# Kernel tuning notes

Hardware: AMD Instinct MI355X
Metric: run time of the kernel (lower is better)

Reference implementation:

```python
import jax, jax.numpy as jnp
import numpy as np

# Model config (matches init_kwargs)
E, TOP_K, H, I = 16, 2, 2048, 1024
B, S = 2, 2048
GROUP = 16                 # NVFP4 quantization group size along contraction dim
RSF = 1.0                  # routed_scaling_factor


def setup_inputs() -> dict:
    key = jax.random.key(0)
    ks = jax.random.split(key, 6)
    hidden_states = jax.random.normal(ks[0], (B, S, H), dtype=jnp.float32)
    gate_weight = jax.random.normal(ks[1], (E, H), dtype=jnp.float32) * 0.02
    # int4 codes stored as int32 in [0,16); reference subtracts 8 -> [-8,7]
    fc_up_qweights = jax.random.randint(ks[2], (E, H, I), 0, 16, dtype=jnp.int32)
    fc_up_blocks_scale = jax.random.uniform(ks[3], (E, H // GROUP, I), dtype=jnp.float32) * 0.02
    fc_up_global_scale = jnp.ones((1,), dtype=jnp.float32)
    fc_down_qweights = jax.random.randint(ks[4], (E, I, H), 0, 16, dtype=jnp.int32)
    fc_down_blocks_scale = jax.random.uniform(ks[5], (E, I // GROUP, H), dtype=jnp.float32) * 0.02
    fc_down_global_scale = jnp.ones((1,), dtype=jnp.float32)
    return {
        'hidden_states': hidden_states,
        'gate_weight': gate_weight,
        'fc_up_blocks_scale': fc_up_blocks_scale,
        'fc_up_global_scale': fc_up_global_scale,
        'fc_down_blocks_scale': fc_down_blocks_scale,
        'fc_down_global_scale': fc_down_global_scale,
        'fc_up_qweights': fc_up_qweights,
        'fc_down_qweights': fc_down_qweights,
    }


def _dequant(q, blocks_scale, global_scale):
    # q: [E,K,N] int codes (0..15 -> -8..7); blocks_scale: [E,K/GROUP,N]
    e, k, n = q.shape
    w = (q.astype(jnp.float32) - 8.0).reshape(e, k // GROUP, GROUP, n)
    w = w * blocks_scale[:, :, None, :]
    return w.reshape(e, k, n) * global_scale[0]


def reference(hidden_states, gate_weight, fc_up_blocks_scale, fc_up_global_scale,
              fc_down_blocks_scale, fc_down_global_scale,
              fc_up_qweights, fc_down_qweights):
    b, s, h = hidden_states.shape
    x = hidden_states.reshape(-1, h).astype(jnp.float32)          # [T,H]
    t = x.shape[0]

    # Router: HF sigmoid routing mapped through logsigmoid so that
    # softmax(logsigmoid(l)) == sigmoid(l)/sum(sigmoid(l))  (nemotron_h_plugin_router_logits)
    logits = jax.nn.log_sigmoid(x @ gate_weight.T)                # [T,E]
    probs = jax.nn.softmax(logits, axis=-1)
    topw, topi = jax.lax.top_k(probs, TOP_K)                      # [T,K]
    topw = topw / (jnp.sum(topw, axis=-1, keepdims=True) + 1e-20) # renormalize

    # Dense per-token expert weights [T,E] (scatter of top-k weights)
    wdense = jnp.zeros((t, E), dtype=jnp.float32)
    wdense = wdense.at[jnp.arange(t)[:, None], topi].add(topw) * RSF

    w_up = _dequant(fc_up_qweights, fc_up_blocks_scale, fc_up_global_scale)     # [E,H,I]
    w_down = _dequant(fc_down_qweights, fc_down_blocks_scale, fc_down_global_scale)  # [E,I,H]

    z = jnp.einsum('th,ehi->tei', x, w_up)                        # up proj
    a = jnp.square(jnp.maximum(z, 0.0))                           # activation_type=0: ReLU^2
    aw = a * wdense[:, :, None]                                   # fold routing weights (linear)
    y = jnp.einsum('tei,eih->th', aw, w_down)                     # down proj + combine
    return y.reshape(b, s, h)
```

## Files before the change

kernel.cpp:

```cpp
#include <hip/hip_runtime.h>

#define TOK 4096
#define NE 16
#define HD 2048
#define ID 1024
#define QGROUP 16
#define CAP 4096

typedef _Float16 half4v __attribute__((ext_vector_type(4)));
typedef _Float16 half8v __attribute__((ext_vector_type(8)));
typedef float float4v __attribute__((ext_vector_type(4)));

__device__ __forceinline__ float bf2f(unsigned int u) { return __uint_as_float(u << 16); }

__global__ __launch_bounds__(256) void prep_kernel(
    const float* __restrict__ x, _Float16* __restrict__ xh)
{
    int i8 = (blockIdx.x * 256 + threadIdx.x) * 8;
    float4 f0 = *(const float4*)&x[i8];
    float4 f1 = *(const float4*)&x[i8 + 4];
    half8v h;
    h[0] = (_Float16)f0.x; h[1] = (_Float16)f0.y; h[2] = (_Float16)f0.z; h[3] = (_Float16)f0.w;
    h[4] = (_Float16)f1.x; h[5] = (_Float16)f1.y; h[6] = (_Float16)f1.z; h[7] = (_Float16)f1.w;
    *(half8v*)&xh[i8] = h;
}

__global__ __launch_bounds__(256) void router_kernel(
    const float* __restrict__ x, const float* __restrict__ gw,
    int* __restrict__ counts, int* __restrict__ pair_row, float* __restrict__ pair_w)
{
    int t = blockIdx.x;
    int tid = threadIdx.x;
    float p[NE];
#pragma unroll
    for (int e = 0; e < NE; e++) p[e] = 0.f;
    const float* xr = x + (size_t)t * HD;
    for (int h = tid; h < HD; h += 256) {
        float xv = xr[h];
#pragma unroll
        for (int e = 0; e < NE; e++) p[e] = fmaf(xv, gw[e * HD + h], p[e]);
    }
#pragma unroll
    for (int off = 32; off > 0; off >>= 1) {
#pragma unroll
        for (int e = 0; e < NE; e++) p[e] += __shfl_down(p[e], off, 64);
    }
    __shared__ float part[4][NE];
    int wave = tid >> 6, lane = tid & 63;
    if (lane == 0) {
#pragma unroll
        for (int e = 0; e < NE; e++) part[wave][e] = p[e];
    }
    __syncthreads();
    if (tid == 0) {
        float s[NE]; float sum = 0.f;
#pragma unroll
        for (int e = 0; e < NE; e++) {
            float l = part[0][e] + part[1][e] + part[2][e] + part[3][e];
            float sg = 1.f / (1.f + expf(-l));
            s[e] = sg; sum += sg;
        }
        int i1 = 0;
#pragma unroll
        for (int e = 1; e < NE; e++) if (s[e] > s[i1]) i1 = e;
        int i2 = (i1 == 0) ? 1 : 0;
#pragma unroll
        for (int e = 0; e < NE; e++) if (e != i1 && s[e] > s[i2]) i2 = e;
        float p1 = s[i1] / sum, p2 = s[i2] / sum;
        float inv = 1.f / (p1 + p2 + 1e-20f);
        float w1 = p1 * inv, w2 = p2 * inv;
        int s1 = atomicAdd(&counts[i1], 1);
        pair_row[i1 * CAP + s1] = t * 2;     pair_w[i1 * CAP + s1] = w1;
        int s2 = atomicAdd(&counts[i2], 1);
        pair_row[i2 * CAP + s2] = t * 2 + 1; pair_w[i2 * CAP + s2] = w2;
    }
}

template<int N, int K, bool UP>
__global__ __launch_bounds__(256) void gemm_kernel(
    const _Float16* __restrict__ A, const int* __restrict__ qw,
    const float* __restrict__ bsc, const float* __restrict__ gsc,
    const int* __restrict__ counts, const int* __restrict__ pair_row,
    const float* __restrict__ pair_w,
    _Float16* __restrict__ store16, float* __restrict__ store32)
{
    constexpr int NT = N / 128;
    const int e = blockIdx.y;
    const int cnt = counts[e];
    const int mt = blockIdx.x / NT, nt = blockIdx.x % NT;
    const int mbase = mt * 128;
    if (mbase >= cnt) return;
    const int nbase = nt * 128;
    const int tid = threadIdx.x;

    __shared__ _Float16 As[128][40];
    __shared__ _Float16 Bs[128][40];
    __shared__ int rows_s[128];
    __shared__ float pw_s[128];

    if (tid < 128) {
        int idx = mbase + tid; if (idx >= cnt) idx = cnt - 1;
        rows_s[tid] = pair_row[e * CAP + idx];
        pw_s[tid] = UP ? pair_w[e * CAP + idx] : 0.f;
    }

    const int lane = tid & 63, wv = tid >> 6;
    const int quad = lane >> 4, lm = lane & 15;
    const int wr = (wv >> 1) * 64, wc = (wv & 1) * 64;

    float4v acc[4][4];
#pragma unroll
    for (int mi = 0; mi < 4; mi++)
#pragma unroll
        for (int ni = 0; ni < 4; ni++) acc[mi][ni] = (float4v){0.f, 0.f, 0.f, 0.f};

    const int am = tid & 127, akk = (tid >> 7) * 16;
    const int bn4 = (tid & 31) * 4, bkb = (tid >> 5) * 4;

    for (int k0 = 0; k0 < K; k0 += 32) {
        __syncthreads();
        {
            int pr = rows_s[am];
            int row = UP ? (pr >> 1) : pr;
            const _Float16* src = A + (size_t)row * K + k0 + akk;
            uint4 r0 = *(const uint4*)src;
            uint4 r1 = *(const uint4*)(src + 8);
            *(uint4*)&As[am][akk] = r0;
            *(uint4*)&As[am][akk + 8] = r1;
        }
        {
            const int kabs = k0 + bkb;
            const int g = kabs >> 4;
            const float4 sc = *(const float4*)&bsc[((size_t)e * (K / QGROUP) + g) * N + nbase + bn4];
            const int4 c0 = *(const int4*)&qw[((size_t)e * K + kabs + 0) * N + nbase + bn4];
            const int4 c1 = *(const int4*)&qw[((size_t)e * K + kabs + 1) * N + nbase + bn4];
            const int4 c2 = *(const int4*)&qw[((size_t)e * K + kabs + 2) * N + nbase + bn4];
            const int4 c3 = *(const int4*)&qw[((size_t)e * K + kabs + 3) * N + nbase + bn4];
            half4v q;
            q[0] = (_Float16)((c0.x - 8) * sc.x); q[1] = (_Float16)((c1.x - 8) * sc.x);
            q[2] = (_Float16)((c2.x - 8) * sc.x); q[3] = (_Float16)((c3.x - 8) * sc.x);
            *(half4v*)&Bs[bn4 + 0][bkb] = q;
            q[0] = (_Float16)((c0.y - 8) * sc.y); q[1] = (_Float16)((c1.y - 8) * sc.y);
            q[2] = (_Float16)((c2.y - 8) * sc.y); q[3] = (_Float16)((c3.y - 8) * sc.y);
            *(half4v*)&Bs[bn4 + 1][bkb] = q;
            q[0] = (_Float16)((c0.z - 8) * sc.z); q[1] = (_Float16)((c1.z - 8) * sc.z);
            q[2] = (_Float16)((c2.z - 8) * sc.z); q[3] = (_Float16)((c3.z - 8) * sc.z);
            *(half4v*)&Bs[bn4 + 2][bkb] = q;
            q[0] = (_Float16)((c0.w - 8) * sc.w); q[1] = (_Float16)((c1.w - 8) * sc.w);
            q[2] = (_Float16)((c2.w - 8) * sc.w); q[3] = (_Float16)((c3.w - 8) * sc.w);
            *(half4v*)&Bs[bn4 + 3][bkb] = q;
        }
        __syncthreads();
        half8v af[4], bf[4];
#pragma unroll
        for (int mi = 0; mi < 4; mi++)
            af[mi] = *(const half8v*)&As[wr + mi * 16 + lm][quad * 8];
#pragma unroll
        for (int ni = 0; ni < 4; ni++)
            bf[ni] = *(const half8v*)&Bs[wc + ni * 16 + lm][quad * 8];
#pragma unroll
        for (int mi = 0; mi < 4; mi++)
#pragma unroll
            for (int ni = 0; ni < 4; ni++)
                acc[mi][ni] = __builtin_amdgcn_mfma_f32_16x16x32_f16(af[mi], bf[ni], acc[mi][ni], 0, 0, 0);
    }

    const float gs = gsc[0];
#pragma unroll
    for (int mi = 0; mi < 4; mi++) {
#pragma unroll
        for (int r = 0; r < 4; r++) {
            const int rl = wr + mi * 16 + quad * 4 + r;
            const int grow = mbase + rl;
            if (grow < cnt) {
                const int pr = rows_s[rl];
#pragma unroll
                for (int ni = 0; ni < 4; ni++) {
                    const int col = nbase + wc + ni * 16 + lm;
                    float v = acc[mi][ni][r] * gs;
                    if (UP) {
                        v = fmaxf(v, 0.f);
                        v = v * v * pw_s[rl];
                        store16[(size_t)pr * N + col] = (_Float16)v;
                    } else if (store16) {
                        store16[(size_t)pr * N + col] = (_Float16)v;
                    } else {
                        atomicAdd(&store32[(size_t)(pr >> 1) * N + col], v);
                    }
                }
            }
        }
    }
}

__global__ __launch_bounds__(256) void finalize_kernel(
    const _Float16* __restrict__ ydown, float* __restrict__ out)
{
    int i = (blockIdx.x * 256 + threadIdx.x) * 4;
    int t = i >> 11;
    int h = i & 2047;
    size_t a = ((size_t)t << 12) + h;
    half4v ra = *(const half4v*)&ydown[a];
    half4v rb = *(const half4v*)&ydown[a + HD];
    float4 o;
    o.x = (float)ra[0] + (float)rb[0];
    o.y = (float)ra[1] + (float)rb[1];
    o.z = (float)ra[2] + (float)rb[2];
    o.w = (float)ra[3] + (float)rb[3];
    *(float4*)&out[i] = o;
}

extern "C" void kernel_launch(void* const* d_in, const int* in_sizes, int n_in,
                              void* d_out, int out_size, void* d_ws, size_t ws_size,
                              hipStream_t stream) {
    const float* x   = (const float*)d_in[0];
    const float* gw  = (const float*)d_in[1];
    const float* usc = (const float*)d_in[2];
    const float* ugs = (const float*)d_in[3];
    const float* dsc = (const float*)d_in[4];
    const float* dgs = (const float*)d_in[5];
    const int*   uq  = (const int*)d_in[6];
    const int*   dq  = (const int*)d_in[7];
    float* out = (float*)d_out;

    char* ws = (char*)d_ws;
    int*   counts   = (int*)(ws + 0);
    int*   pair_row = (int*)(ws + 4096);
    float* pair_w   = (float*)(ws + 4096 + (size_t)NE * CAP * 4);
    _Float16* xh    = (_Float16*)(ws + 528384);
    _Float16* act   = (_Float16*)(ws + 528384 + (size_t)TOK * HD * 2);
    _Float16* ydown = (_Float16*)(ws + 528384 + (size_t)TOK * HD * 2
                                  + (size_t)2 * TOK * ID * 2);
    const size_t need_ydown = 34082816ull + (size_t)2 * TOK * HD * 2;
    const bool use_ydown = ws_size >= need_ydown;

    hipMemsetAsync(counts, 0, 4096, stream);
    if (!use_ydown) hipMemsetAsync(out, 0, (size_t)TOK * HD * 4, stream);

    prep_kernel<<<(TOK * HD) / (256 * 8), 256, 0, stream>>>(x, xh);
    router_kernel<<<TOK, 256, 0, stream>>>(x, gw, counts, pair_row, pair_w);
    gemm_kernel<ID, HD, true><<<dim3((CAP / 128) * (ID / 128), NE), 256, 0, stream>>>(
        xh, uq, usc, ugs, counts, pair_row, pair_w, act, nullptr);
    gemm_kernel<HD, ID, false><<<dim3((CAP / 128) * (HD / 128), NE), 256, 0, stream>>>(
        act, dq, dsc, dgs, counts, pair_row, pair_w,
        use_ydown ? ydown : nullptr, use_ydown ? nullptr : out);
    if (use_ydown)
        finalize_kernel<<<(TOK * HD) / 1024, 256, 0, stream>>>(ydown, out);
}
```

Baseline: 605.4 us.

## Prefetch next K-tile into registers and reshape grouped GEMM tiles to 64x128x64

The grouped MoE GEMM now loads the next K-step's activations, int4 codes and scales into registers before running the current step's MFMAs, so global latency overlaps compute. The tile changes from 128x128 with K-step 32 to 64 rows by 128 columns with K-step 64, and the grid is doubled along M. Each thread now dequantizes 8 K values per column and writes them as half8 vectors. In exchange, each weight tile is reloaded by twice as many blocks, and register pressure rises from the prefetch buffers.

```diff
diff --git a/kernel.cpp b/kernel.cpp
--- a/kernel.cpp
+++ b/kernel.cpp
@@ -10,8 +10,6 @@
 typedef _Float16 half4v __attribute__((ext_vector_type(4)));
 typedef _Float16 half8v __attribute__((ext_vector_type(8)));
 typedef float float4v __attribute__((ext_vector_type(4)));
-
-__device__ __forceinline__ float bf2f(unsigned int u) { return __uint_as_float(u << 16); }
 
 __global__ __launch_bounds__(256) void prep_kernel(
     const float* __restrict__ x, _Float16* __restrict__ xh)
@@ -88,95 +86,109 @@
     const int e = blockIdx.y;
     const int cnt = counts[e];
     const int mt = blockIdx.x / NT, nt = blockIdx.x % NT;
-    const int mbase = mt * 128;
+    const int mbase = mt * 64;
     if (mbase >= cnt) return;
     const int nbase = nt * 128;
     const int tid = threadIdx.x;
 
-    __shared__ _Float16 As[128][40];
-    __shared__ _Float16 Bs[128][40];
-    __shared__ int rows_s[128];
-    __shared__ float pw_s[128];
-
-    if (tid < 128) {
+    __shared__ _Float16 As[64][68];
+    __shared__ _Float16 Bs[128][68];
+    __shared__ int rows_s[64];
+    __shared__ float pw_s[64];
+
+    if (tid < 64) {
         int idx = mbase + tid; if (idx >= cnt) idx = cnt - 1;
         rows_s[tid] = pair_row[e * CAP + idx];
         pw_s[tid] = UP ? pair_w[e * CAP + idx] : 0.f;
     }
+    __syncthreads();
+
+    const int arow = tid & 63;
+    const int aseg = (tid >> 6) * 16;
+    const int pr_a = rows_s[arow];
+    const _Float16* asrc = A + (size_t)(UP ? (pr_a >> 1) : pr_a) * K + aseg;
+
+    const int bn4 = (tid & 31) * 4;
+    const int bkb = (tid >> 5) * 8;
+    const int* bsrc = qw + ((size_t)e * K + bkb) * N + nbase + bn4;
+    const float* ssrc = bsc + ((size_t)e * (K / QGROUP) + (bkb >> 4)) * N + nbase + bn4;
+
+    uint4 pa0 = *(const uint4*)asrc;
+    uint4 pa1 = *(const uint4*)(asrc + 8);
+    int4 pc[8];
+#pragma unroll
+    for (int j = 0; j < 8; j++) pc[j] = *(const int4*)(bsrc + (size_t)j * N);
+    float4 psc = *(const float4*)ssrc;
 
     const int lane = tid & 63, wv = tid >> 6;
     const int quad = lane >> 4, lm = lane & 15;
-    const int wr = (wv >> 1) * 64, wc = (wv & 1) * 64;
-
-    float4v acc[4][4];
-#pragma unroll
-    for (int mi = 0; mi < 4; mi++)
+    const int wm = (wv & 1) * 32, wn = (wv >> 1) * 64;
+
+    float4v acc[2][4];
+#pragma unroll
+    for (int mi = 0; mi < 2; mi++)
 #pragma unroll
         for (int ni = 0; ni < 4; ni++) acc[mi][ni] = (float4v){0.f, 0.f, 0.f, 0.f};
 
-    const int am = tid & 127, akk = (tid >> 7) * 16;
-    const int bn4 = (tid & 31) * 4, bkb = (tid >> 5) * 4;
-
-    for (int k0 = 0; k0 < K; k0 += 32) {
+    for (int k0 = 0; k0 < K; k0 += 64) {
         __syncthreads();
+        *(uint4*)&As[arow][aseg] = pa0;
+        *(uint4*)&As[arow][aseg + 8] = pa1;
         {
-            int pr = rows_s[am];
-            int row = UP ? (pr >> 1) : pr;
-            const _Float16* src = A + (size_t)row * K + k0 + akk;
-            uint4 r0 = *(const uint4*)src;
-            uint4 r1 = *(const uint4*)(src + 8);
-            *(uint4*)&As[am][akk] = r0;
-            *(uint4*)&As[am][akk + 8] = r1;
-        }
-        {
-            const int kabs = k0 + bkb;
-            const int g = kabs >> 4;
-            const float4 sc = *(const float4*)&bsc[((size_t)e * (K / QGROUP) + g) * N + nbase + bn4];
-            const int4 c0 = *(const int4*)&qw[((size_t)e * K + kabs + 0) * N + nbase + bn4];
-            const int4 c1 = *(const int4*)&qw[((size_t)e * K + kabs + 1) * N + nbase + bn4];
-            const int4 c2 = *(const int4*)&qw[((size_t)e * K + kabs + 2) * N + nbase + bn4];
-            const int4 c3 = *(const int4*)&qw[((size_t)e * K + kabs + 3) * N + nbase + bn4];
-            half4v q;
-            q[0] = (_Float16)((c0.x - 8) * sc.x); q[1] = (_Float16)((c1.x - 8) * sc.x);
-            q[2] = (_Float16)((c2.x - 8) * sc.x); q[3] = (_Float16)((c3.x - 8) * sc.x);
-            *(half4v*)&Bs[bn4 + 0][bkb] = q;
-            q[0] = (_Float16)((c0.y - 8) * sc.y); q[1] = (_Float16)((c1.y - 8) * sc.y);
-            q[2] = (_Float16)((c2.y - 8) * sc.y); q[3] = (_Float16)((c3.y - 8) * sc.y);
-            *(half4v*)&Bs[bn4 + 1][bkb] = q;
-            q[0] = (_Float16)((c0.z - 8) * sc.z); q[1] = (_Float16)((c1.z - 8) * sc.z);
-            q[2] = (_Float16)((c2.z - 8) * sc.z); q[3] = (_Float16)((c3.z - 8) * sc.z);
-            *(half4v*)&Bs[bn4 + 2][bkb] = q;
-            q[0] = (_Float16)((c0.w - 8) * sc.w); q[1] = (_Float16)((c1.w - 8) * sc.w);
-            q[2] = (_Float16)((c2.w - 8) * sc.w); q[3] = (_Float16)((c3.w - 8) * sc.w);
-            *(half4v*)&Bs[bn4 + 3][bkb] = q;
+            half8v h0, h1, h2, h3;
+#pragma unroll
+            for (int j = 0; j < 8; j++) {
+                h0[j] = (_Float16)((float)(pc[j].x - 8) * psc.x);
+                h1[j] = (_Float16)((float)(pc[j].y - 8) * psc.y);
+                h2[j] = (_Float16)((float)(pc[j].z - 8) * psc.z);
+                h3[j] = (_Float16)((float)(pc[j].w - 8) * psc.w);
+            }
+            *(half8v*)&Bs[bn4 + 0][bkb] = h0;
+            *(half8v*)&Bs[bn4 + 1][bkb] = h1;
+            *(half8v*)&Bs[bn4 + 2][bkb] = h2;
+            *(half8v*)&Bs[bn4 + 3][bkb] = h3;
         }
         __syncthreads();
-        half8v af[4], bf[4];
-#pragma unroll
-        for (int mi = 0; mi < 4; mi++)
-            af[mi] = *(const half8v*)&As[wr + mi * 16 + lm][quad * 8];
-#pragma unroll
-        for (int ni = 0; ni < 4; ni++)
-            bf[ni] = *(const half8v*)&Bs[wc + ni * 16 + lm][quad * 8];
-#pragma unroll
-        for (int mi = 0; mi < 4; mi++)
+        if (k0 + 64 < K) {
+            asrc += 64;
+            pa0 = *(const uint4*)asrc;
+            pa1 = *(const uint4*)(asrc + 8);
+            bsrc += (size_t)64 * N;
+#pragma unroll
+            for (int j = 0; j < 8; j++) pc[j] = *(const int4*)(bsrc + (size_t)j * N);
+            ssrc += (size_t)4 * N;
+            psc = *(const float4*)ssrc;
+        }
+        half8v af[2][2], bf[2][4];
+#pragma unroll
+        for (int ks = 0; ks < 2; ks++) {
+#pragma unroll
+            for (int mi = 0; mi < 2; mi++)
+                af[ks][mi] = *(const half8v*)&As[wm + mi * 16 + lm][ks * 32 + quad * 8];
 #pragma unroll
             for (int ni = 0; ni < 4; ni++)
-                acc[mi][ni] = __builtin_amdgcn_mfma_f32_16x16x32_f16(af[mi], bf[ni], acc[mi][ni], 0, 0, 0);
+                bf[ks][ni] = *(const half8v*)&Bs[wn + ni * 16 + lm][ks * 32 + quad * 8];
+        }
+#pragma unroll
+        for (int ks = 0; ks < 2; ks++)
+#pragma unroll
+            for (int mi = 0; mi < 2; mi++)
+#pragma unroll
+                for (int ni = 0; ni < 4; ni++)
+                    acc[mi][ni] = __builtin_amdgcn_mfma_f32_16x16x32_f16(af[ks][mi], bf[ks][ni], acc[mi][ni], 0, 0, 0);
     }
 
     const float gs = gsc[0];
 #pragma unroll
-    for (int mi = 0; mi < 4; mi++) {
+    for (int mi = 0; mi < 2; mi++) {
 #pragma unroll
         for (int r = 0; r < 4; r++) {
-            const int rl = wr + mi * 16 + quad * 4 + r;
-            const int grow = mbase + rl;
-            if (grow < cnt) {
+            const int rl = wm + mi * 16 + quad * 4 + r;
+            if (mbase + rl < cnt) {
                 const int pr = rows_s[rl];
 #pragma unroll
                 for (int ni = 0; ni < 4; ni++) {
-                    const int col = nbase + wc + ni * 16 + lm;
+                    const int col = nbase + wn + ni * 16 + lm;
                     float v = acc[mi][ni][r] * gs;
                     if (UP) {
                         v = fmaxf(v, 0.f);
@@ -239,9 +251,9 @@
 
     prep_kernel<<<(TOK * HD) / (256 * 8), 256, 0, stream>>>(x, xh);
     router_kernel<<<TOK, 256, 0, stream>>>(x, gw, counts, pair_row, pair_w);
-    gemm_kernel<ID, HD, true><<<dim3((CAP / 128) * (ID / 128), NE), 256, 0, stream>>>(
+    gemm_kernel<ID, HD, true><<<dim3((CAP / 64) * (ID / 128), NE), 256, 0, stream>>>(
         xh, uq, usc, ugs, counts, pair_row, pair_w, act, nullptr);
-    gemm_kernel<HD, ID, false><<<dim3((CAP / 128) * (HD / 128), NE), 256, 0, stream>>>(
+    gemm_kernel<HD, ID, false><<<dim3((CAP / 64) * (HD / 128), NE), 256, 0, stream>>>(
         act, dq, dsc, dgs, counts, pair_row, pair_w,
         use_ydown ? ydown : nullptr, use_ydown ? nullptr : out);
     if (use_ydown)
```

Result: slower. 635.1 us (+4.9%).

## Pre-dequantize weights to transposed fp16 and stream tiles via global_load_lds

Applied to the files above, without the earlier changes.

Adds a separate kernel that dequantizes each expert's int32 int4 codes into a transposed fp16 weight buffer in workspace, one projection at a time. A new GEMM then loads A and B tiles with direct global-to-LDS 16-byte loads instead of dequantizing inside the main loop. The down projection now always accumulates into the output with fp32 atomics, replacing the fp16 per-pair buffer and its finalize pass. This trades an extra full pass over the weights (read int32, write fp16) for a much leaner GEMM inner loop. The new path has no LDS padding and no double buffering, so bank conflicts and load latency may still limit it.

```diff
diff --git a/kernel.cpp b/kernel.cpp
--- a/kernel.cpp
+++ b/kernel.cpp
@@ -11,7 +11,11 @@
 typedef _Float16 half8v __attribute__((ext_vector_type(8)));
 typedef float float4v __attribute__((ext_vector_type(4)));
 
-__device__ __forceinline__ float bf2f(unsigned int u) { return __uint_as_float(u << 16); }
+__device__ __forceinline__ void g2l16(const void* g, void* l) {
+    __builtin_amdgcn_global_load_lds(
+        (const __attribute__((address_space(1))) unsigned int*)g,
+        (__attribute__((address_space(3))) unsigned int*)l, 16, 0, 0);
+}
 
 __global__ __launch_bounds__(256) void prep_kernel(
     const float* __restrict__ x, _Float16* __restrict__ xh)
@@ -76,10 +80,46 @@
     }
 }
 
+template<int K, int N>
+__global__ __launch_bounds__(256) void dequantT_kernel(
+    const int* __restrict__ qw, const float* __restrict__ bsc, _Float16* __restrict__ wq)
+{
+    const int e = blockIdx.z, kt = blockIdx.y, nt = blockIdx.x;
+    const int tid = threadIdx.x;
+    __shared__ _Float16 T[64][68];
+
+    const int c4 = (tid & 15) * 4;
+    const int r0 = tid >> 4;
+#pragma unroll
+    for (int p = 0; p < 4; p++) {
+        const int r = p * 16 + r0;
+        const int kabs = kt * 64 + r;
+        const int4 c = *(const int4*)&qw[((size_t)e * K + kabs) * N + nt * 64 + c4];
+        const float4 sc = *(const float4*)&bsc[((size_t)e * (K / QGROUP) + (kabs >> 4)) * N + nt * 64 + c4];
+        half4v h;
+        h[0] = (_Float16)((float)(c.x - 8) * sc.x);
+        h[1] = (_Float16)((float)(c.y - 8) * sc.y);
+        h[2] = (_Float16)((float)(c.z - 8) * sc.z);
+        h[3] = (_Float16)((float)(c.w - 8) * sc.w);
+        *(half4v*)&T[r][c4] = h;
+    }
+    __syncthreads();
+    const int nrow = tid >> 2;
+    const int kseg = (tid & 3) * 16;
+    half8v o0, o1;
+#pragma unroll
+    for (int i = 0; i < 8; i++) o0[i] = T[kseg + i][nrow];
+#pragma unroll
+    for (int i = 0; i < 8; i++) o1[i] = T[kseg + 8 + i][nrow];
+    _Float16* dst = wq + ((size_t)e * N + nt * 64 + nrow) * K + kt * 64 + kseg;
+    *(half8v*)dst = o0;
+    *(half8v*)(dst + 8) = o1;
+}
+
 template<int N, int K, bool UP>
-__global__ __launch_bounds__(256) void gemm_kernel(
-    const _Float16* __restrict__ A, const int* __restrict__ qw,
-    const float* __restrict__ bsc, const float* __restrict__ gsc,
+__global__ __launch_bounds__(256) void gemm2_kernel(
+    const _Float16* __restrict__ A, const _Float16* __restrict__ BT,
+    const float* __restrict__ gsc,
     const int* __restrict__ counts, const int* __restrict__ pair_row,
     const float* __restrict__ pair_w,
     _Float16* __restrict__ store16, float* __restrict__ store32)
@@ -93,6 +133,108 @@
     const int nbase = nt * 128;
     const int tid = threadIdx.x;
 
+    __shared__ _Float16 As[128 * 32];
+    __shared__ _Float16 Bs[128 * 32];
+    __shared__ int rows_s[128];
+    __shared__ float pw_s[128];
+
+    if (tid < 128) {
+        int idx = mbase + tid; if (idx >= cnt) idx = cnt - 1;
+        rows_s[tid] = pair_row[e * CAP + idx];
+        pw_s[tid] = UP ? pair_w[e * CAP + idx] : 0.f;
+    }
+    __syncthreads();
+
+    const int lane = tid & 63, wv = tid >> 6;
+    const int quad = lane >> 4, lm = lane & 15;
+    const int wr = (wv >> 1) * 64, wc = (wv & 1) * 64;
+
+    const int lsub = lane >> 2;
+    const int lkof = (lane & 3) * 8;
+    const _Float16* asrc[2];
+    const _Float16* bsrc[2];
+    _Float16* adst[2];
+    _Float16* bdst[2];
+#pragma unroll
+    for (int i = 0; i < 2; i++) {
+        const int lr = wv * 32 + i * 16 + lsub;
+        const int pr = rows_s[lr];
+        asrc[i] = A + (size_t)(UP ? (pr >> 1) : pr) * K + lkof;
+        bsrc[i] = BT + ((size_t)e * N + nbase + lr) * K + lkof;
+        adst[i] = &As[(wv * 32 + i * 16) * 32];
+        bdst[i] = &Bs[(wv * 32 + i * 16) * 32];
+    }
+
+    float4v acc[4][4];
+#pragma unroll
+    for (int mi = 0; mi < 4; mi++)
+#pragma unroll
+        for (int ni = 0; ni < 4; ni++) acc[mi][ni] = (float4v){0.f, 0.f, 0.f, 0.f};
+
+    for (int k0 = 0; k0 < K; k0 += 32) {
+#pragma unroll
+        for (int i = 0; i < 2; i++) {
+            g2l16(asrc[i] + k0, adst[i]);
+            g2l16(bsrc[i] + k0, bdst[i]);
+        }
+        __syncthreads();
+        half8v af[4], bf[4];
+#pragma unroll
+        for (int mi = 0; mi < 4; mi++)
+            af[mi] = *(const half8v*)&As[(wr + mi * 16 + lm) * 32 + quad * 8];
+#pragma unroll
+        for (int ni = 0; ni < 4; ni++)
+            bf[ni] = *(const half8v*)&Bs[(wc + ni * 16 + lm) * 32 + quad * 8];
+#pragma unroll
+        for (int mi = 0; mi < 4; mi++)
+#pragma unroll
+            for (int ni = 0; ni < 4; ni++)
+                acc[mi][ni] = __builtin_amdgcn_mfma_f32_16x16x32_f16(af[mi], bf[ni], acc[mi][ni], 0, 0, 0);
+        __syncthreads();
+    }
+
+    const float gs = gsc[0];
+#pragma unroll
+    for (int mi = 0; mi < 4; mi++) {
+#pragma unroll
+        for (int r = 0; r < 4; r++) {
+            const int rl = wr + mi * 16 + quad * 4 + r;
+            if (mbase + rl < cnt) {
+                const int pr = rows_s[rl];
+#pragma unroll
+                for (int ni = 0; ni < 4; ni++) {
+                    const int col = nbase + wc + ni * 16 + lm;
+                    float v = acc[mi][ni][r] * gs;
+                    if (UP) {
+                        v = fmaxf(v, 0.f);
+                        v = v * v * pw_s[rl];
+                        store16[(size_t)pr * N + col] = (_Float16)v;
+                    } else {
+                        atomicAdd(&store32[(size_t)(pr >> 1) * N + col], v);
+                    }
+                }
+            }
+        }
+    }
+}
+
+template<int N, int K, bool UP>
+__global__ __launch_bounds__(256) void gemm_fused_kernel(
+    const _Float16* __restrict__ A, const int* __restrict__ qw,
+    const float* __restrict__ bsc, const float* __restrict__ gsc,
+    const int* __restrict__ counts, const int* __restrict__ pair_row,
+    const float* __restrict__ pair_w,
+    _Float16* __restrict__ store16, float* __restrict__ store32)
+{
+    constexpr int NT = N / 128;
+    const int e = blockIdx.y;
+    const int cnt = counts[e];
+    const int mt = blockIdx.x / NT, nt = blockIdx.x % NT;
+    const int mbase = mt * 128;
+    if (mbase >= cnt) return;
+    const int nbase = nt * 128;
+    const int tid = threadIdx.x;
+
     __shared__ _Float16 As[128][40];
     __shared__ _Float16 Bs[128][40];
     __shared__ int rows_s[128];
@@ -121,17 +263,13 @@
         __syncthreads();
         {
             int pr = rows_s[am];
-            int row = UP ? (pr >> 1) : pr;
-            const _Float16* src = A + (size_t)row * K + k0 + akk;
-            uint4 r0 = *(const uint4*)src;
-            uint4 r1 = *(const uint4*)(src + 8);
-            *(uint4*)&As[am][akk] = r0;
-            *(uint4*)&As[am][akk + 8] = r1;
+            const _Float16* src = A + (size_t)(UP ? (pr >> 1) : pr) * K + k0 + akk;
+            *(uint4*)&As[am][akk] = *(const uint4*)src;
+            *(uint4*)&As[am][akk + 8] = *(const uint4*)(src + 8);
         }
         {
             const int kabs = k0 + bkb;
-            const int g = kabs >> 4;
-            const float4 sc = *(const float4*)&bsc[((size_t)e * (K / QGROUP) + g) * N + nbase + bn4];
+            const float4 sc = *(const float4*)&bsc[((size_t)e * (K / QGROUP) + (kabs >> 4)) * N + nbase + bn4];
             const int4 c0 = *(const int4*)&qw[((size_t)e * K + kabs + 0) * N + nbase + bn4];
             const int4 c1 = *(const int4*)&qw[((size_t)e * K + kabs + 1) * N + nbase + bn4];
             const int4 c2 = *(const int4*)&qw[((size_t)e * K + kabs + 2) * N + nbase + bn4];
@@ -171,8 +309,7 @@
 #pragma unroll
         for (int r = 0; r < 4; r++) {
             const int rl = wr + mi * 16 + quad * 4 + r;
-            const int grow = mbase + rl;
-            if (grow < cnt) {
+            if (mbase + rl < cnt) {
                 const int pr = rows_s[rl];
 #pragma unroll
                 for (int ni = 0; ni < 4; ni++) {
@@ -182,8 +319,6 @@
                         v = fmaxf(v, 0.f);
                         v = v * v * pw_s[rl];
                         store16[(size_t)pr * N + col] = (_Float16)v;
-                    } else if (store16) {
-                        store16[(size_t)pr * N + col] = (_Float16)v;
                     } else {
                         atomicAdd(&store32[(size_t)(pr >> 1) * N + col], v);
                     }
@@ -191,23 +326,6 @@
             }
         }
     }
-}
-
-__global__ __launch_bounds__(256) void finalize_kernel(
-    const _Float16* __restrict__ ydown, float* __restrict__ out)
-{
-    int i = (blockIdx.x * 256 + threadIdx.x) * 4;
-    int t = i >> 11;
-    int h = i & 2047;
-    size_t a = ((size_t)t << 12) + h;
-    half4v ra = *(const half4v*)&ydown[a];
-    half4v rb = *(const half4v*)&ydown[a + HD];
-    float4 o;
-    o.x = (float)ra[0] + (float)rb[0];
-    o.y = (float)ra[1] + (float)rb[1];
-    o.z = (float)ra[2] + (float)rb[2];
-    o.w = (float)ra[3] + (float)rb[3];
-    *(float4*)&out[i] = o;
 }
 
 extern "C" void kernel_launch(void* const* d_in, const int* in_sizes, int n_in,
@@ -229,21 +347,28 @@
     float* pair_w   = (float*)(ws + 4096 + (size_t)NE * CAP * 4);
     _Float16* xh    = (_Float16*)(ws + 528384);
     _Float16* act   = (_Float16*)(ws + 528384 + (size_t)TOK * HD * 2);
-    _Float16* ydown = (_Float16*)(ws + 528384 + (size_t)TOK * HD * 2
+    _Float16* wq    = (_Float16*)(ws + 528384 + (size_t)TOK * HD * 2
                                   + (size_t)2 * TOK * ID * 2);
-    const size_t need_ydown = 34082816ull + (size_t)2 * TOK * HD * 2;
-    const bool use_ydown = ws_size >= need_ydown;
+    const size_t need_deq = 34082816ull + (size_t)NE * HD * ID * 2;
+    const bool use_deq = ws_size >= need_deq;
 
     hipMemsetAsync(counts, 0, 4096, stream);
-    if (!use_ydown) hipMemsetAsync(out, 0, (size_t)TOK * HD * 4, stream);
+    hipMemsetAsync(out, 0, (size_t)TOK * HD * 4, stream);
 
     prep_kernel<<<(TOK * HD) / (256 * 8), 256, 0, stream>>>(x, xh);
     router_kernel<<<TOK, 256, 0, stream>>>(x, gw, counts, pair_row, pair_w);
-    gemm_kernel<ID, HD, true><<<dim3((CAP / 128) * (ID / 128), NE), 256, 0, stream>>>(
-        xh, uq, usc, ugs, counts, pair_row, pair_w, act, nullptr);
-    gemm_kernel<HD, ID, false><<<dim3((CAP / 128) * (HD / 128), NE), 256, 0, stream>>>(
-        act, dq, dsc, dgs, counts, pair_row, pair_w,
-        use_ydown ? ydown : nullptr, use_ydown ? nullptr : out);
-    if (use_ydown)
-        finalize_kernel<<<(TOK * HD) / 1024, 256, 0, stream>>>(ydown, out);
-}
+
+    if (use_deq) {
+        dequantT_kernel<HD, ID><<<dim3(ID / 64, HD / 64, NE), 256, 0, stream>>>(uq, usc, wq);
+        gemm2_kernel<ID, HD, true><<<dim3((CAP / 128) * (ID / 128), NE), 256, 0, stream>>>(
+            xh, wq, ugs, counts, pair_row, pair_w, act, nullptr);
+        dequantT_kernel<ID, HD><<<dim3(HD / 64, ID / 64, NE), 256, 0, stream>>>(dq, dsc, wq);
+        gemm2_kernel<HD, ID, false><<<dim3((CAP / 128) * (HD / 128), NE), 256, 0, stream>>>(
+            act, wq, dgs, counts, pair_row, pair_w, nullptr, out);
+    } else {
+        gemm_fused_kernel<ID, HD, true><<<dim3((CAP / 128) * (ID / 128), NE), 256, 0, stream>>>(
+            xh, uq, usc, ugs, counts, pair_row, pair_w, act, nullptr);
+        gemm_fused_kernel<HD, ID, false><<<dim3((CAP / 128) * (HD / 128), NE), 256, 0, stream>>>(
+            act, dq, dsc, dgs, counts, pair_row, pair_w, nullptr, out);
+    }
+}
```

After: 600.1 us. No clear change (-0.9%).
